# Kernel tuning notes

Measured on AMD Instinct MI355X. Metric: run time of the kernel, lower is better.

Reference implementation:

```python
import jax, jax.numpy as jnp
import numpy as np

B, S, E, H = 4, 2048, 1024, 16
D = E // H  # head_dim = 64


def setup_inputs() -> dict:
    key = jax.random.key(0)
    ks = jax.random.split(key, 10)
    scale = 1.0 / np.sqrt(E)
    return {
        "decoder_sequence": jax.random.normal(ks[0], (B, S, E), dtype=jnp.float32),
        # stacked per-head projection weights (math-equivalent to per-head nn.Linear)
        "Wq": jax.random.normal(ks[1], (H, E, D), dtype=jnp.float32) * scale,
        "bq": jnp.zeros((H, D), dtype=jnp.float32),
        "Wk": jax.random.normal(ks[2], (H, E, D), dtype=jnp.float32) * scale,
        "bk": jnp.zeros((H, D), dtype=jnp.float32),
        "Wv": jax.random.normal(ks[3], (H, E, D), dtype=jnp.float32) * scale,
        "bv": jnp.zeros((H, D), dtype=jnp.float32),
        "Wo": jax.random.normal(ks[4], (E, E), dtype=jnp.float32) * scale,
        "bo": jnp.zeros((E,), dtype=jnp.float32),
    }


def reference(decoder_sequence, Wq, bq, Wk, bk, Wv, bv, Wo, bo):
    x = decoder_sequence  # [B,S,E]
    # per-head Q/K/V projections, batched over the head axis
    Q = jnp.einsum('bse,hed->bhsd', x, Wq) + bq[:, None, :]
    K = jnp.einsum('bse,hed->bhsd', x, Wk) + bk[:, None, :]
    V = jnp.einsum('bse,hed->bhsd', x, Wv) + bv[:, None, :]
    # scaled scores with causal mask (upper triangle -> -inf)
    A = jnp.einsum('bhid,bhjd->bhij', Q, K) / jnp.sqrt(jnp.float32(D))
    causal = jnp.tril(jnp.ones((S, S), dtype=bool))  # True where allowed
    A = jnp.where(causal, A, -jnp.inf)
    A = jax.nn.softmax(A, axis=-1)
    Hout = jnp.einsum('bhij,bhjd->bhid', A, V)  # [B,H,S,D]
    # concat heads: [B,S,H*D]
    concat = jnp.transpose(Hout, (0, 2, 1, 3)).reshape(B, S, H * D)
    return concat @ Wo.T + bo
```

## Files before the change

### kernel.cpp

```cpp
#include <hip/hip_runtime.h>
#include <stdint.h>
#include <stddef.h>

typedef __bf16 bf16;
typedef __bf16 bf16x8 __attribute__((ext_vector_type(8)));
typedef __bf16 bf16x4 __attribute__((ext_vector_type(4)));
typedef float  f32x4  __attribute__((ext_vector_type(4)));
typedef float  f32x16 __attribute__((ext_vector_type(16)));
typedef unsigned short ush;
typedef ush ush8 __attribute__((ext_vector_type(8)));
typedef unsigned int uint;

#define B_  4
#define S_  2048
#define E_  1024
#define H_  16
#define D_  64
#define M_  (B_*S_)
#define K_  E_
#define QSCALE 0.18033688011112042f

__device__ __forceinline__ void gload_lds16(const void* g, void* l) {
  __builtin_amdgcn_global_load_lds((const __attribute__((address_space(1))) void*)g,
                                   (__attribute__((address_space(3))) void*)l, 16, 0, 0);
}
__device__ __forceinline__ f32x4 mfma16(bf16x8 a, bf16x8 b, f32x4 c) {
  return __builtin_amdgcn_mfma_f32_16x16x32_bf16(a, b, c, 0, 0, 0);
}
__device__ __forceinline__ f32x16 mfma32(bf16x8 a, bf16x8 b, f32x16 c) {
  return __builtin_amdgcn_mfma_f32_32x32x16_bf16(a, b, c, 0, 0, 0);
}
__device__ __forceinline__ int swz4(int row, int ch) { return ch ^ ((row >> 1) & 3); }
__device__ __forceinline__ uint cvtpk(float lo, float hi) {
  uint r;
  asm("v_cvt_pk_bf16_f32 %0, %1, %2" : "=v"(r) : "v"(lo), "v"(hi));
  return r;
}

__global__ void cast_f32_bf16(const float* __restrict__ src, bf16* __restrict__ dst, int n4) {
  int idx = blockIdx.x * blockDim.x + threadIdx.x;
  int stride = gridDim.x * blockDim.x;
  for (int i = idx; i < n4; i += stride) {
    float4 v = ((const float4*)src)[i];
    union { bf16 b[4]; ushort4 u; } cv;
    cv.b[0] = (bf16)v.x; cv.b[1] = (bf16)v.y; cv.b[2] = (bf16)v.z; cv.b[3] = (bf16)v.w;
    ((ushort4*)dst)[i] = cv.u;
  }
}

__global__ void pack_w_t(const float* __restrict__ Wq, const float* __restrict__ Wk,
                         const float* __restrict__ Wv, bf16* __restrict__ Wp) {
  __shared__ float t[64][65];
  const int tid = threadIdx.x;
  const int wh = blockIdx.y;
  const int which = wh >> 4, h = wh & 15;
  const int e0 = blockIdx.x << 6;
  const float* src = (which == 0) ? Wq : (which == 1 ? Wk : Wv);
  src += (size_t)h * (E_ * D_);
  #pragma unroll
  for (int i = 0; i < 4; ++i) {
    int fi = tid + 256 * i;
    int e = fi >> 4, c = fi & 15;
    float4 v = *(const float4*)(src + (size_t)(e0 + e) * D_ + c * 4);
    t[c * 4 + 0][e] = v.x; t[c * 4 + 1][e] = v.y;
    t[c * 4 + 2][e] = v.z; t[c * 4 + 3][e] = v.w;
  }
  __syncthreads();
  #pragma unroll
  for (int i = 0; i < 2; ++i) {
    int cid = tid + 256 * i;
    int d = cid >> 3, cc = cid & 7;
    ush8 o;
    #pragma unroll
    for (int j = 0; j < 8; ++j) {
      union { bf16 b; ush u; } cv; cv.b = (bf16)t[d][cc * 8 + j]; o[j] = cv.u;
    }
    *(ush8*)(Wp + ((size_t)which * 1024 + h * 64 + d) * K_ + e0 + cc * 8) = o;
  }
}

template <int MODE>
__launch_bounds__(256, 2)
__global__ void gemm_kernel(const bf16* __restrict__ A, const bf16* __restrict__ Bm,
                            int Ntot,
                            const float* __restrict__ bias0, const float* __restrict__ bias1,
                            const float* __restrict__ bias2,
                            bf16* __restrict__ Qo, bf16* __restrict__ Ko, bf16* __restrict__ Vto,
                            float* __restrict__ Fo) {
  __shared__ __align__(16) bf16 lds_a[2][128 * 32];
  __shared__ __align__(16) bf16 lds_b[2][128 * 32];
  const int tid = threadIdx.x;
  const int lane = tid & 63;
  const int w = tid >> 6;
  const int wr = w >> 1, wc = w & 1;
  const int nblk = Ntot >> 7;
  const int qch = gridDim.x >> 3;
  const int swz = (blockIdx.x & 7) * qch + (blockIdx.x >> 3);
  const int mt = swz / nblk, nt = swz % nblk;
  const int m0 = mt << 7, n0 = nt << 7;

  f32x4 acc[4][4] = {};

  auto stage = [&](int buf, int kt) {
    #pragma unroll
    for (int i = 0; i < 2; ++i) {
      int cb = (w * 2 + i) * 64;
      int cid = cb + lane;
      int row = cid >> 2, cir = cid & 3;
      int lch = swz4(row, cir);
      const bf16* ga = A  + (size_t)(m0 + row) * K_ + kt * 32 + lch * 8;
      const bf16* gb = Bm + (size_t)(n0 + row) * K_ + kt * 32 + lch * 8;
      gload_lds16(ga, &lds_a[buf][cb * 8]);
      gload_lds16(gb, &lds_b[buf][cb * 8]);
    }
  };

  const int NT = K_ / 32;
  stage(0, 0);
  for (int kt = 0; kt < NT; ++kt) {
    if (kt + 1 < NT) stage((kt + 1) & 1, kt + 1);
    __syncthreads();
    const bf16x8* pa = (const bf16x8*)&lds_a[kt & 1][0];
    const bf16x8* pb = (const bf16x8*)&lds_b[kt & 1][0];
    bf16x8 af[4], bfr[4];
    #pragma unroll
    for (int mb = 0; mb < 4; ++mb) {
      int row = wr * 64 + mb * 16 + (lane & 15);
      af[mb] = pa[row * 4 + swz4(row, lane >> 4)];
    }
    #pragma unroll
    for (int nb = 0; nb < 4; ++nb) {
      int row = wc * 64 + nb * 16 + (lane & 15);
      bfr[nb] = pb[row * 4 + swz4(row, lane >> 4)];
    }
    #pragma unroll
    for (int mb = 0; mb < 4; ++mb)
      #pragma unroll
      for (int nb = 0; nb < 4; ++nb)
        acc[mb][nb] = mfma16(af[mb], bfr[nb], acc[mb][nb]);
    __syncthreads();
  }

  #pragma unroll
  for (int mb = 0; mb < 4; ++mb) {
    #pragma unroll
    for (int nb = 0; nb < 4; ++nb) {
      const int ni  = n0 + wc * 64 + nb * 16 + (lane & 15);
      const int mi0 = m0 + wr * 64 + mb * 16 + (lane >> 4) * 4;
      if (MODE == 0) {
        const int which = ni >> 10;
        const int col = ni & 1023;
        const float* bp = (which == 0) ? bias0 : (which == 1 ? bias1 : bias2);
        const float bv = bp[col];
        const int hh = col >> 6, d = col & 63;
        const int b = mi0 >> 11, s0r = mi0 & 2047;
        if (which == 2) {
          bf16x4 st;
          #pragma unroll
          for (int r = 0; r < 4; ++r) st[r] = (bf16)(acc[mb][nb][r] + bv);
          *(bf16x4*)(Vto + ((size_t)((b * H_ + hh) * D_ + d)) * S_ + s0r) = st;
        } else {
          bf16* dst = (which == 0) ? Qo : Ko;
          const float sc = (which == 0) ? QSCALE : 1.f;
          #pragma unroll
          for (int r = 0; r < 4; ++r)
            dst[(((size_t)(b * H_ + hh)) * S_ + (s0r + r)) * D_ + d] =
                (bf16)((acc[mb][nb][r] + bv) * sc);
        }
      } else {
        #pragma unroll
        for (int r = 0; r < 4; ++r)
          Fo[(size_t)(mi0 + r) * E_ + ni] = acc[mb][nb][r] + bias0[ni];
      }
    }
  }
}

struct QTile {
  bf16x8 qf[4];
  f32x16 oacc[2];
  float m, l;
};

__device__ __forceinline__ void init_q(QTile& S, const bf16* qrow, int hi) {
  #pragma unroll
  for (int kc = 0; kc < 4; ++kc)
    S.qf[kc] = *(const bf16x8*)(qrow + (2 * kc + hi) * 8);
  #pragma unroll
  for (int r = 0; r < 16; ++r) { S.oacc[0][r] = 0.f; S.oacc[1][r] = 0.f; }
  S.m = -1e30f; S.l = 0.f;
}

__device__ __forceinline__ void tile_step(QTile& S, const bf16* klds, const bf16* vlds,
                                          int kv0, int qb_, int qg_, int hi, int ln) {
  if (kv0 > qb_ + 31) return;
  f32x16 s0 = {}, s1 = {};
  #pragma unroll
  for (int kc = 0; kc < 4; ++kc) {
    int ch = (2 * kc + hi) ^ (ln & 7);
    bf16x8 k0 = *(const bf16x8*)&klds[ln * 64 + ch * 8];
    bf16x8 k1 = *(const bf16x8*)&klds[(32 + ln) * 64 + ch * 8];
    s0 = mfma32(k0, S.qf[kc], s0);
    s1 = mfma32(k1, S.qf[kc], s1);
  }
  if (kv0 + 63 > qb_) {
    #pragma unroll
    for (int r = 0; r < 16; ++r) {
      int crow = (r & 3) + 8 * (r >> 2) + 4 * hi;
      if (kv0 + crow > qg_)      s0[r] = -1e30f;
      if (kv0 + 32 + crow > qg_) s1[r] = -1e30f;
    }
  }
  float mt_ = s0[0];
  #pragma unroll
  for (int r = 1; r < 16; ++r) mt_ = fmaxf(mt_, s0[r]);
  #pragma unroll
  for (int r = 0; r < 16; ++r) mt_ = fmaxf(mt_, s1[r]);
  mt_ = fmaxf(mt_, __shfl_xor(mt_, 32, 64));
  bool resc = mt_ > S.m + 8.f;
  float mnew = resc ? mt_ : S.m;
  float alpha = resc ? exp2f(S.m - mnew) : 1.f;
  S.m = mnew;
  float rs = 0.f;
  #pragma unroll
  for (int r = 0; r < 16; ++r) { float p = exp2f(s0[r] - mnew); s0[r] = p; rs += p; }
  #pragma unroll
  for (int r = 0; r < 16; ++r) { float p = exp2f(s1[r] - mnew); s1[r] = p; rs += p; }
  rs += __shfl_xor(rs, 32, 64);
  S.l = S.l * alpha + rs;
  if (__any(resc)) {
    #pragma unroll
    for (int r = 0; r < 16; ++r) { S.oacc[0][r] *= alpha; S.oacc[1][r] *= alpha; }
  }
  bf16x8 pf[4];
  #pragma unroll
  for (int mtl = 0; mtl < 2; ++mtl) {
    #pragma unroll
    for (int c = 0; c < 2; ++c) {
      const f32x16& p = mtl ? s1 : s0;
      uint wa = cvtpk(p[8 * c + 0], p[8 * c + 1]);
      uint wb = cvtpk(p[8 * c + 2], p[8 * c + 3]);
      uint wcx = cvtpk(p[8 * c + 4], p[8 * c + 5]);
      uint wd = cvtpk(p[8 * c + 6], p[8 * c + 7]);
      asm("v_permlane32_swap_b32 %0, %1" : "+v"(wa), "+v"(wcx));
      asm("v_permlane32_swap_b32 %0, %1" : "+v"(wb), "+v"(wd));
      union { uint u[4]; bf16x8 v; } cvt;
      cvt.u[0] = wa; cvt.u[1] = wb; cvt.u[2] = wcx; cvt.u[3] = wd;
      pf[mtl * 2 + c] = cvt.v;
    }
  }
  #pragma unroll
  for (int dm = 0; dm < 2; ++dm) {
    #pragma unroll
    for (int ks = 0; ks < 4; ++ks) {
      int row = dm * 32 + ln;
      int ch = (2 * ks + hi) ^ (ln & 7);
      bf16x8 vf = *(const bf16x8*)&vlds[row * 64 + ch * 8];
      S.oacc[dm] = mfma32(vf, pf[ks], S.oacc[dm]);
    }
  }
}

__device__ __forceinline__ void store_o(const QTile& S, bf16* orow, int hi) {
  float rinv = 1.f / S.l;
  #pragma unroll
  for (int dm = 0; dm < 2; ++dm) {
    #pragma unroll
    for (int g = 0; g < 4; ++g) {
      bf16x4 st;
      #pragma unroll
      for (int i = 0; i < 4; ++i) st[i] = (bf16)(S.oacc[dm][4 * g + i] * rinv);
      *(bf16x4*)(orow + dm * 32 + g * 8 + hi * 4) = st;
    }
  }
}

__device__ __forceinline__ void store_part(const QTile& S, bf16* prow, float* pml, int hi) {
  #pragma unroll
  for (int dm = 0; dm < 2; ++dm) {
    #pragma unroll
    for (int g = 0; g < 4; ++g) {
      bf16x4 st;
      #pragma unroll
      for (int i = 0; i < 4; ++i) st[i] = (bf16)S.oacc[dm][4 * g + i];
      *(bf16x4*)(prow + dm * 32 + g * 8 + hi * 4) = st;
    }
  }
  if (hi == 0) { pml[0] = S.m; pml[1] = S.l; }
}

__launch_bounds__(256, 2)
__global__ void attn_kernel(const bf16* __restrict__ Q, const bf16* __restrict__ K,
                            const bf16* __restrict__ Vt, bf16* __restrict__ Cc,
                            bf16* __restrict__ Po, float* __restrict__ Pml, int nh) {
  __shared__ __align__(16) bf16 k_lds[2][64 * 64];
  __shared__ __align__(16) bf16 v_lds[2][64 * 64];
  const int tid = threadIdx.x, lane = tid & 63, w = tid >> 6;
  const int hi = lane >> 5, ln = lane & 31;
  const int bid = blockIdx.x;
  const int bh = bid & 63;
  const int rest = bid >> 6;
  const int x = rest & 7;
  const int h = (nh == 2) ? (rest >> 3) : 0;
  const int jta = x, jtb = 15 - x;
  const int lenA = (2 * x + 2) / nh, lenB = (32 - 2 * x) / nh;
  const int ta0 = h * lenA, ta1 = ta0 + lenA;
  const int tb0 = h * lenB, tb1 = tb0 + lenB;
  const bf16* Kb = K  + (size_t)bh * (S_ * D_);
  const bf16* Vb = Vt + (size_t)bh * (D_ * S_);

  auto stage = [&](int buf, int t) {
    const int kv0 = t << 6;
    #pragma unroll
    for (int i = 0; i < 2; ++i) {
      int cb = (w * 2 + i) * 64;
      int cid = cb + lane;
      int row = cid >> 3, cir = cid & 7;
      int lch = cir ^ (row & 7);
      gload_lds16(Kb + (size_t)(kv0 + row) * D_ + lch * 8, &k_lds[buf][cb * 8]);
      gload_lds16(Vb + (size_t)row * S_ + kv0 + lch * 8, &v_lds[buf][cb * 8]);
    }
  };

  QTile SA, SB;
  const int sA = jta * 128 + w * 32 + ln, sB = jtb * 128 + w * 32 + ln;
  init_q(SA, Q + ((size_t)bh * S_ + sA) * D_, hi);
  init_q(SB, Q + ((size_t)bh * S_ + sB) * D_, hi);

  {
    const int qb_ = jta * 128 + w * 32, qg_ = qb_ + ln;
    stage(0, ta0);
    __syncthreads();
    for (int t = ta0; t < ta1; ++t) {
      int cur = (t - ta0) & 1;
      if (t + 1 < ta1) stage(cur ^ 1, t + 1);
      tile_step(SA, k_lds[cur], v_lds[cur], t * 64, qb_, qg_, hi, ln);
      __syncthreads();
    }
  }
  {
    const int qb_ = jtb * 128 + w * 32, qg_ = qb_ + ln;
    stage(0, tb0);
    __syncthreads();
    for (int t = tb0; t < tb1; ++t) {
      int cur = (t - tb0) & 1;
      if (t + 1 < tb1) stage(cur ^ 1, t + 1);
      tile_step(SB, k_lds[cur], v_lds[cur], t * 64, qb_, qg_, hi, ln);
      __syncthreads();
    }
  }

  if (nh == 2) {
    size_t ra = (size_t)(h * 64 + bh) * 2048 + sA;
    size_t rb = (size_t)(h * 64 + bh) * 2048 + sB;
    store_part(SA, Po + ra * 64, Pml + ra * 2, hi);
    store_part(SB, Po + rb * 64, Pml + rb * 2, hi);
  } else {
    const int b = bh >> 4, hh = bh & 15;
    store_o(SA, Cc + ((size_t)(b * S_ + sA)) * E_ + hh * D_, hi);
    store_o(SB, Cc + ((size_t)(b * S_ + sB)) * E_ + hh * D_, hi);
  }
}

__global__ void attn_merge(const bf16* __restrict__ Po, const float* __restrict__ Pml,
                           bf16* __restrict__ Cc) {
  const int idx = blockIdx.x * 256 + threadIdx.x;
  const int rg = idx >> 3, oct = idx & 7;
  const int bh = rg >> 11, s = rg & 2047;
  const size_t r0 = (size_t)bh * 2048 + s;
  const size_t r1 = (size_t)(64 + bh) * 2048 + s;
  const float m0 = Pml[r0 * 2], l0 = Pml[r0 * 2 + 1];
  const float m1 = Pml[r1 * 2], l1 = Pml[r1 * 2 + 1];
  const float mx = fmaxf(m0, m1);
  const float a0 = exp2f(m0 - mx), a1 = exp2f(m1 - mx);
  const float rl = 1.f / (l0 * a0 + l1 * a1);
  const bf16x8 v0 = *(const bf16x8*)(Po + r0 * 64 + oct * 8);
  const bf16x8 v1 = *(const bf16x8*)(Po + r1 * 64 + oct * 8);
  bf16x8 o;
  #pragma unroll
  for (int j = 0; j < 8; ++j)
    o[j] = (bf16)(((float)v0[j] * a0 + (float)v1[j] * a1) * rl);
  const int b = bh >> 4, hh = bh & 15;
  *(bf16x8*)(Cc + ((size_t)(b * S_ + s)) * E_ + hh * D_ + oct * 8) = o;
}

extern "C" void kernel_launch(void* const* d_in, const int* in_sizes, int n_in,
                              void* d_out, int out_size, void* d_ws, size_t ws_size,
                              hipStream_t stream) {
  const float* x  = (const float*)d_in[0];
  const float* Wq = (const float*)d_in[1];
  const float* bq = (const float*)d_in[2];
  const float* Wk = (const float*)d_in[3];
  const float* bk = (const float*)d_in[4];
  const float* Wv = (const float*)d_in[5];
  const float* bv = (const float*)d_in[6];
  const float* Wo = (const float*)d_in[7];
  const float* bo = (const float*)d_in[8];
  float* out = (float*)d_out;

  uint8_t* ws = (uint8_t*)d_ws;
  bf16* Xbf   = (bf16*)(ws + 0);
  bf16* Wpack = (bf16*)(ws + 16777216);
  bf16* Wot   = (bf16*)(ws + 23068672);
  bf16* Qb    = (bf16*)(ws + 25165824);
  bf16* Kb    = (bf16*)(ws + 41943040);
  bf16* Vtb   = (bf16*)(ws + 75497472);
  bf16* Cc    = Xbf;
  bf16*  Po  = (bf16*)(ws + 92274688);
  float* Pml = (float*)(ws + 125829120);
  const bool split = (ws_size >= 127926272ull);
  const int nh = split ? 2 : 1;

  cast_f32_bf16<<<2048, 256, 0, stream>>>(x,  Xbf, (M_ * K_) / 4);
  cast_f32_bf16<<<1024, 256, 0, stream>>>(Wo, Wot, (E_ * E_) / 4);
  pack_w_t<<<dim3(16, 48), 256, 0, stream>>>(Wq, Wk, Wv, Wpack);

  gemm_kernel<0><<<dim3(64 * 24), 256, 0, stream>>>(Xbf, Wpack, 3072, bq, bk, bv,
                                                    Qb, Kb, Vtb, nullptr);

  attn_kernel<<<dim3(512 * nh), 256, 0, stream>>>(Qb, Kb, Vtb, Cc, Po, Pml, nh);
  if (split) attn_merge<<<dim3(4096), 256, 0, stream>>>(Po, Pml, Cc);

  gemm_kernel<1><<<dim3(64 * 8), 256, 0, stream>>>(Cc, Wot, 1024, bo, nullptr, nullptr,
                                                   nullptr, nullptr, nullptr, out);
}
```

Measured before the change: 199.9 us.

## Stage 128-row KV tiles in attention, drop split-KV merge, raise GEMM occupancy

The attention kernel now loads 128 KV rows per pipeline phase (two 64-row sub-steps per barrier) into larger LDS buffers, with a 16-way XOR swizzle for the wider V tile. This halves the number of syncs and stage calls. The split-KV path, which wrote partial results and ran a separate merge kernel, is removed, so attention always writes the final output directly from 512 blocks. The GEMM launch bound goes to 3 blocks per CU. The trade-offs are fewer blocks (512) for attention parallelism, double the LDS per block, and possible register pressure in the GEMM.

Measured after the change: 189.3 us. 1.06x faster.

```diff
diff --git a/kernel.cpp b/kernel.cpp
--- a/kernel.cpp
+++ b/kernel.cpp
@@ -80,7 +80,7 @@
 }
 
 template <int MODE>
-__launch_bounds__(256, 2)
+__launch_bounds__(256, 3)
 __global__ void gemm_kernel(const bf16* __restrict__ A, const bf16* __restrict__ Bm,
                             int Ntot,
                             const float* __restrict__ bias0, const float* __restrict__ bias1,
@@ -192,14 +192,15 @@
 }
 
 __device__ __forceinline__ void tile_step(QTile& S, const bf16* klds, const bf16* vlds,
-                                          int kv0, int qb_, int qg_, int hi, int ln) {
+                                          int sub, int kv0, int qb_, int qg_, int hi, int ln) {
   if (kv0 > qb_ + 31) return;
+  const bf16* kbase = klds + sub * (64 * 64);
   f32x16 s0 = {}, s1 = {};
   #pragma unroll
   for (int kc = 0; kc < 4; ++kc) {
     int ch = (2 * kc + hi) ^ (ln & 7);
-    bf16x8 k0 = *(const bf16x8*)&klds[ln * 64 + ch * 8];
-    bf16x8 k1 = *(const bf16x8*)&klds[(32 + ln) * 64 + ch * 8];
+    bf16x8 k0 = *(const bf16x8*)&kbase[ln * 64 + ch * 8];
+    bf16x8 k1 = *(const bf16x8*)&kbase[(32 + ln) * 64 + ch * 8];
     s0 = mfma32(k0, S.qf[kc], s0);
     s1 = mfma32(k1, S.qf[kc], s1);
   }
@@ -254,8 +255,9 @@
     #pragma unroll
     for (int ks = 0; ks < 4; ++ks) {
       int row = dm * 32 + ln;
-      int ch = (2 * ks + hi) ^ (ln & 7);
-      bf16x8 vf = *(const bf16x8*)&vlds[row * 64 + ch * 8];
+      int cfull = sub * 8 + 2 * ks + hi;
+      int ch = cfull ^ (ln & 15);
+      bf16x8 vf = *(const bf16x8*)&vlds[row * 128 + ch * 8];
       S.oacc[dm] = mfma32(vf, pf[ks], S.oacc[dm]);
     }
   }
@@ -275,113 +277,68 @@
   }
 }
 
-__device__ __forceinline__ void store_part(const QTile& S, bf16* prow, float* pml, int hi) {
-  #pragma unroll
-  for (int dm = 0; dm < 2; ++dm) {
-    #pragma unroll
-    for (int g = 0; g < 4; ++g) {
-      bf16x4 st;
-      #pragma unroll
-      for (int i = 0; i < 4; ++i) st[i] = (bf16)S.oacc[dm][4 * g + i];
-      *(bf16x4*)(prow + dm * 32 + g * 8 + hi * 4) = st;
-    }
-  }
-  if (hi == 0) { pml[0] = S.m; pml[1] = S.l; }
-}
-
 __launch_bounds__(256, 2)
 __global__ void attn_kernel(const bf16* __restrict__ Q, const bf16* __restrict__ K,
-                            const bf16* __restrict__ Vt, bf16* __restrict__ Cc,
-                            bf16* __restrict__ Po, float* __restrict__ Pml, int nh) {
-  __shared__ __align__(16) bf16 k_lds[2][64 * 64];
-  __shared__ __align__(16) bf16 v_lds[2][64 * 64];
+                            const bf16* __restrict__ Vt, bf16* __restrict__ Cc) {
+  __shared__ __align__(16) bf16 k_lds[2][128 * 64];
+  __shared__ __align__(16) bf16 v_lds[2][64 * 128];
   const int tid = threadIdx.x, lane = tid & 63, w = tid >> 6;
   const int hi = lane >> 5, ln = lane & 31;
   const int bid = blockIdx.x;
   const int bh = bid & 63;
-  const int rest = bid >> 6;
-  const int x = rest & 7;
-  const int h = (nh == 2) ? (rest >> 3) : 0;
+  const int x = bid >> 6;
   const int jta = x, jtb = 15 - x;
-  const int lenA = (2 * x + 2) / nh, lenB = (32 - 2 * x) / nh;
-  const int ta0 = h * lenA, ta1 = ta0 + lenA;
-  const int tb0 = h * lenB, tb1 = tb0 + lenB;
   const bf16* Kb = K  + (size_t)bh * (S_ * D_);
   const bf16* Vb = Vt + (size_t)bh * (D_ * S_);
-
-  auto stage = [&](int buf, int t) {
-    const int kv0 = t << 6;
-    #pragma unroll
-    for (int i = 0; i < 2; ++i) {
-      int cb = (w * 2 + i) * 64;
+  const int b = bh >> 4, hh = bh & 15;
+
+  auto stage2 = [&](int buf, int ph) {
+    const int kv0 = ph << 7;
+    #pragma unroll
+    for (int i = 0; i < 4; ++i) {
+      int cb = (w * 4 + i) * 64;
       int cid = cb + lane;
       int row = cid >> 3, cir = cid & 7;
       int lch = cir ^ (row & 7);
       gload_lds16(Kb + (size_t)(kv0 + row) * D_ + lch * 8, &k_lds[buf][cb * 8]);
-      gload_lds16(Vb + (size_t)row * S_ + kv0 + lch * 8, &v_lds[buf][cb * 8]);
+      int rowv = cid >> 4, cirv = cid & 15;
+      int lchv = cirv ^ (rowv & 15);
+      gload_lds16(Vb + (size_t)rowv * S_ + kv0 + lchv * 8, &v_lds[buf][cb * 8]);
     }
   };
-
-  QTile SA, SB;
-  const int sA = jta * 128 + w * 32 + ln, sB = jtb * 128 + w * 32 + ln;
-  init_q(SA, Q + ((size_t)bh * S_ + sA) * D_, hi);
-  init_q(SB, Q + ((size_t)bh * S_ + sB) * D_, hi);
 
   {
     const int qb_ = jta * 128 + w * 32, qg_ = qb_ + ln;
-    stage(0, ta0);
+    QTile SA;
+    init_q(SA, Q + ((size_t)bh * S_ + qg_) * D_, hi);
+    const int nph = x + 1;
+    stage2(0, 0);
     __syncthreads();
-    for (int t = ta0; t < ta1; ++t) {
-      int cur = (t - ta0) & 1;
-      if (t + 1 < ta1) stage(cur ^ 1, t + 1);
-      tile_step(SA, k_lds[cur], v_lds[cur], t * 64, qb_, qg_, hi, ln);
+    for (int ph = 0; ph < nph; ++ph) {
+      int cur = ph & 1;
+      if (ph + 1 < nph) stage2(cur ^ 1, ph + 1);
+      tile_step(SA, k_lds[cur], v_lds[cur], 0, ph * 128,      qb_, qg_, hi, ln);
+      tile_step(SA, k_lds[cur], v_lds[cur], 1, ph * 128 + 64, qb_, qg_, hi, ln);
       __syncthreads();
     }
+    store_o(SA, Cc + ((size_t)(b * S_ + qg_)) * E_ + hh * D_, hi);
   }
   {
     const int qb_ = jtb * 128 + w * 32, qg_ = qb_ + ln;
-    stage(0, tb0);
+    QTile SB;
+    init_q(SB, Q + ((size_t)bh * S_ + qg_) * D_, hi);
+    const int nph = 16 - x;
+    stage2(0, 0);
     __syncthreads();
-    for (int t = tb0; t < tb1; ++t) {
-      int cur = (t - tb0) & 1;
-      if (t + 1 < tb1) stage(cur ^ 1, t + 1);
-      tile_step(SB, k_lds[cur], v_lds[cur], t * 64, qb_, qg_, hi, ln);
+    for (int ph = 0; ph < nph; ++ph) {
+      int cur = ph & 1;
+      if (ph + 1 < nph) stage2(cur ^ 1, ph + 1);
+      tile_step(SB, k_lds[cur], v_lds[cur], 0, ph * 128,      qb_, qg_, hi, ln);
+      tile_step(SB, k_lds[cur], v_lds[cur], 1, ph * 128 + 64, qb_, qg_, hi, ln);
       __syncthreads();
     }
-  }
-
-  if (nh == 2) {
-    size_t ra = (size_t)(h * 64 + bh) * 2048 + sA;
-    size_t rb = (size_t)(h * 64 + bh) * 2048 + sB;
-    store_part(SA, Po + ra * 64, Pml + ra * 2, hi);
-    store_part(SB, Po + rb * 64, Pml + rb * 2, hi);
-  } else {
-    const int b = bh >> 4, hh = bh & 15;
-    store_o(SA, Cc + ((size_t)(b * S_ + sA)) * E_ + hh * D_, hi);
-    store_o(SB, Cc + ((size_t)(b * S_ + sB)) * E_ + hh * D_, hi);
-  }
-}
-
-__global__ void attn_merge(const bf16* __restrict__ Po, const float* __restrict__ Pml,
-                           bf16* __restrict__ Cc) {
-  const int idx = blockIdx.x * 256 + threadIdx.x;
-  const int rg = idx >> 3, oct = idx & 7;
-  const int bh = rg >> 11, s = rg & 2047;
-  const size_t r0 = (size_t)bh * 2048 + s;
-  const size_t r1 = (size_t)(64 + bh) * 2048 + s;
-  const float m0 = Pml[r0 * 2], l0 = Pml[r0 * 2 + 1];
-  const float m1 = Pml[r1 * 2], l1 = Pml[r1 * 2 + 1];
-  const float mx = fmaxf(m0, m1);
-  const float a0 = exp2f(m0 - mx), a1 = exp2f(m1 - mx);
-  const float rl = 1.f / (l0 * a0 + l1 * a1);
-  const bf16x8 v0 = *(const bf16x8*)(Po + r0 * 64 + oct * 8);
-  const bf16x8 v1 = *(const bf16x8*)(Po + r1 * 64 + oct * 8);
-  bf16x8 o;
-  #pragma unroll
-  for (int j = 0; j < 8; ++j)
-    o[j] = (bf16)(((float)v0[j] * a0 + (float)v1[j] * a1) * rl);
-  const int b = bh >> 4, hh = bh & 15;
-  *(bf16x8*)(Cc + ((size_t)(b * S_ + s)) * E_ + hh * D_ + oct * 8) = o;
+    store_o(SB, Cc + ((size_t)(b * S_ + qg_)) * E_ + hh * D_, hi);
+  }
 }
 
 extern "C" void kernel_launch(void* const* d_in, const int* in_sizes, int n_in,
@@ -406,10 +363,6 @@
   bf16* Kb    = (bf16*)(ws + 41943040);
   bf16* Vtb   = (bf16*)(ws + 75497472);
   bf16* Cc    = Xbf;
-  bf16*  Po  = (bf16*)(ws + 92274688);
-  float* Pml = (float*)(ws + 125829120);
-  const bool split = (ws_size >= 127926272ull);
-  const int nh = split ? 2 : 1;
 
   cast_f32_bf16<<<2048, 256, 0, stream>>>(x,  Xbf, (M_ * K_) / 4);
   cast_f32_bf16<<<1024, 256, 0, stream>>>(Wo, Wot, (E_ * E_) / 4);
@@ -418,8 +371,7 @@
   gemm_kernel<0><<<dim3(64 * 24), 256, 0, stream>>>(Xbf, Wpack, 3072, bq, bk, bv,
                                                     Qb, Kb, Vtb, nullptr);
 
-  attn_kernel<<<dim3(512 * nh), 256, 0, stream>>>(Qb, Kb, Vtb, Cc, Po, Pml, nh);
-  if (split) attn_merge<<<dim3(4096), 256, 0, stream>>>(Po, Pml, Cc);
+  attn_kernel<<<dim3(512), 256, 0, stream>>>(Qb, Kb, Vtb, Cc);
 
   gemm_kernel<1><<<dim3(64 * 8), 256, 0, stream>>>(Cc, Wot, 1024, bo, nullptr, nullptr,
                                                    nullptr, nullptr, nullptr, out);
```
